# Performance work log

Measured on AMD Instinct MI355X. Metric: run time of the kernel, lower is better.

## Reference

```python
import jax, jax.numpy as jnp
import numpy as np

B, N, F_DIM = 32, 1024, 128
ALPHA = 0.2        # LeakyReLU negative slope
PAD = -9e15        # pad_sequence padding value in the original
DENSITY = 0.05


def setup_inputs() -> dict:
    key = jax.random.key(0)
    k1, k2, k3 = jax.random.split(key, 3)
    # sparse 0/1 adjacency with self-loops so every node has degree >= 1
    adj = (jax.random.uniform(k1, (B, N, N)) < DENSITY).astype(jnp.float32)
    eye = jnp.eye(N, dtype=jnp.float32)[None, :, :]
    adj = jnp.maximum(adj, eye)
    feats = jax.random.normal(k2, (B, N, F_DIM), dtype=jnp.float32)
    # xavier_uniform with leaky_relu gain on a [2F, 1]
    gain = float(np.sqrt(2.0 / (1.0 + ALPHA ** 2)))
    bound = gain * float(np.sqrt(6.0 / (2 * F_DIM + 1)))
    a = jax.random.uniform(k3, (2 * F_DIM, 1), minval=-bound, maxval=bound,
                           dtype=jnp.float32)
    return {"batch_graphs": adj, "batch_features": feats, "a": a}


def reference(batch_graphs, batch_features, a):
    # e_ij = LeakyReLU([h_i || h_j] @ a) decomposes as (h_i @ a1) + (h_j @ a2)
    s_src = batch_features @ a[:F_DIM, 0]   # [B, N] contribution of node i
    s_dst = batch_features @ a[F_DIM:, 0]   # [B, N] contribution of neighbor j
    e = s_src[:, :, None] + s_dst[:, None, :]            # [B, N, N]
    e = jnp.where(e >= 0, e, ALPHA * e)                   # LeakyReLU
    mask = batch_graphs == 1
    e = jnp.where(mask, e, PAD)                           # pad non-edges like pad_sequence
    att = jax.nn.softmax(e, axis=-1)                      # segmented softmax over neighbors
    att = jnp.where(mask, att, 0.0)                       # scatter back only real edges
    return att
```

## Files before the change

kernel.cpp:

```cpp
#include <hip/hip_runtime.h>
#include <hip/hip_bf16.h>
#include <stdint.h>

#define B_DIM 32
#define N_DIM 1024
#define F_DIM 128
#define ALPHA 0.2f
#define NROWS (B_DIM * N_DIM)
#define TAIL_ROWS 128
#define MAIN_ROWS (NROWS - TAIL_ROWS)
#define SCORE_BYTES ((size_t)(2 * NROWS) * sizeof(float))

typedef float          vf4 __attribute__((ext_vector_type(4)));
typedef unsigned short vh4 __attribute__((ext_vector_type(4)));

__device__ __forceinline__ unsigned short f32_to_bf16_bits(float f) {
    union { __hip_bfloat16 h; unsigned short u; } cvt;
    cvt.h = __float2bfloat16(f);
    return cvt.u;
}

__device__ __forceinline__ bool probe_is_f32(const void* adj) {
    return *(const uint32_t*)adj == 0x3F800000u;
}

template <bool F32>
__device__ __forceinline__ float* score_base(void* out) {
    const size_t out_bytes = (size_t)NROWS * N_DIM * (F32 ? 4 : 2);
    return (float*)((char*)out + out_bytes - SCORE_BYTES);
}

template <bool F32>
__device__ __forceinline__ void scores_body(
    const void* __restrict__ feats_v, const void* __restrict__ a_v, void* out)
{
    float* base  = score_base<F32>(out);
    float* s_src = base;
    float* s_dst = base + NROWS;

    const int wid  = threadIdx.x >> 6;
    const int lane = threadIdx.x & 63;
    const int row  = blockIdx.x * 4 + wid;
    const int f0   = lane * 2;

    float x0, x1, a10, a11, a20, a21;
    if (F32) {
        const float* fp = (const float*)feats_v + (size_t)row * F_DIM + f0;
        const float* ap = (const float*)a_v;
        x0 = fp[0]; x1 = fp[1];
        a10 = ap[f0];         a11 = ap[f0 + 1];
        a20 = ap[F_DIM + f0]; a21 = ap[F_DIM + f0 + 1];
    } else {
        const __hip_bfloat16* fp = (const __hip_bfloat16*)feats_v + (size_t)row * F_DIM + f0;
        const __hip_bfloat16* ap = (const __hip_bfloat16*)a_v;
        x0  = __bfloat162float(fp[0]);           x1  = __bfloat162float(fp[1]);
        a10 = __bfloat162float(ap[f0]);          a11 = __bfloat162float(ap[f0 + 1]);
        a20 = __bfloat162float(ap[F_DIM + f0]);  a21 = __bfloat162float(ap[F_DIM + f0 + 1]);
    }

    float v1 = x0 * a10 + x1 * a11;
    float v2 = x0 * a20 + x1 * a21;
    #pragma unroll
    for (int off = 32; off > 0; off >>= 1) {
        v1 += __shfl_down(v1, off, 64);
        v2 += __shfl_down(v2, off, 64);
    }
    if (lane == 0) { s_src[row] = v1; s_dst[row] = v2; }
}

__global__ __launch_bounds__(256) void scores_kernel(
    const void* __restrict__ adj, const void* __restrict__ feats,
    const void* __restrict__ a, void* out)
{
    if (probe_is_f32(adj)) scores_body<true>(feats, a, out);
    else                   scores_body<false>(feats, a, out);
}

template <bool F32>
__device__ __forceinline__ void wave_softmax_row(
    const void* __restrict__ adj_v, void* __restrict__ out_v,
    int row, float ssrc, const float* __restrict__ sdst )
{
    const int lane = threadIdx.x & 63;

    float p[16];
    float lsum = 0.0f;

    #pragma unroll
    for (int c = 0; c < 4; ++c) {
        const int idx = c * 64 + lane;
        const vf4 sd = ((const vf4*)sdst)[idx];
        float av[4];
        if (F32) {
            const vf4 aq = ((const vf4*)((const float*)adj_v + (size_t)row * N_DIM))[idx];
            av[0] = aq.x; av[1] = aq.y; av[2] = aq.z; av[3] = aq.w;
        } else {
            const vh4 aq = ((const vh4*)((const __hip_bfloat16*)adj_v + (size_t)row * N_DIM))[idx];
            av[0] = __uint_as_float((unsigned)aq.x << 16);
            av[1] = __uint_as_float((unsigned)aq.y << 16);
            av[2] = __uint_as_float((unsigned)aq.z << 16);
            av[3] = __uint_as_float((unsigned)aq.w << 16);
        }
        const float sdk[4] = {sd.x, sd.y, sd.z, sd.w};
        #pragma unroll
        for (int k = 0; k < 4; ++k) {
            float t = ssrc + sdk[k];
            t = fmaxf(t, ALPHA * t);
            const float e = __expf(t) * av[k];
            p[c * 4 + k] = e;
            lsum += e;
        }
    }

    #pragma unroll
    for (int off = 1; off < 64; off <<= 1)
        lsum += __shfl_xor(lsum, off, 64);
    const float inv = 1.0f / lsum;

    #pragma unroll
    for (int c = 0; c < 4; ++c) {
        const int idx = c * 64 + lane;
        if (F32) {
            vf4 o;
            o.x = p[c*4+0] * inv; o.y = p[c*4+1] * inv;
            o.z = p[c*4+2] * inv; o.w = p[c*4+3] * inv;
            ((vf4*)((float*)out_v + (size_t)row * N_DIM))[idx] = o;
        } else {
            vh4 o;
            o.x = f32_to_bf16_bits(p[c*4+0] * inv);
            o.y = f32_to_bf16_bits(p[c*4+1] * inv);
            o.z = f32_to_bf16_bits(p[c*4+2] * inv);
            o.w = f32_to_bf16_bits(p[c*4+3] * inv);
            ((vh4*)((__hip_bfloat16*)out_v + (size_t)row * N_DIM))[idx] = o;
        }
    }
}

template <bool F32>
__device__ __forceinline__ void main_body(const void* __restrict__ adj_v, void* out_v)
{
    const int wid = threadIdx.x >> 6;
    const int row = blockIdx.x * 4 + wid;
    const int b   = row >> 10;

    const float* base = score_base<F32>(out_v);
    const float  ssrc = base[row];
    const float* sdst = base + NROWS + (size_t)b * N_DIM;

    wave_softmax_row<F32>(adj_v, out_v, row, ssrc, sdst);
}

__global__ __launch_bounds__(256) void main_kernel(
    const void* __restrict__ adj, void* out)
{
    if (probe_is_f32(adj)) main_body<true>(adj, out);
    else                   main_body<false>(adj, out);
}

template <bool F32>
__device__ __forceinline__ void tail_body(
    const void* __restrict__ adj_v, const void* __restrict__ feats_v,
    const void* __restrict__ a_v, void* __restrict__ out_v)
{
    __shared__ float sdst_sh[N_DIM];

    const int tid  = threadIdx.x;
    const int wid  = tid >> 6;
    const int lane = tid & 63;
    const int b    = B_DIM - 1;
    const int row  = MAIN_ROWS + blockIdx.x * 4 + wid;

    #pragma unroll
    for (int k = 0; k < 4; ++k) {
        const int j = tid * 4 + k;
        float acc = 0.0f;
        if (F32) {
            const vf4* fp = (const vf4*)((const float*)feats_v + ((size_t)b * N_DIM + j) * F_DIM);
            const vf4* ap = (const vf4*)((const float*)a_v + F_DIM);
            #pragma unroll 8
            for (int f = 0; f < F_DIM / 4; ++f) {
                const vf4 x = fp[f], w = ap[f];
                acc += x.x * w.x + x.y * w.y + x.z * w.z + x.w * w.w;
            }
        } else {
            const __hip_bfloat16* fp = (const __hip_bfloat16*)feats_v + ((size_t)b * N_DIM + j) * F_DIM;
            const __hip_bfloat16* ap = (const __hip_bfloat16*)a_v + F_DIM;
            #pragma unroll 8
            for (int f = 0; f < F_DIM; ++f)
                acc += __bfloat162float(fp[f]) * __bfloat162float(ap[f]);
        }
        sdst_sh[j] = acc;
    }

    float ssrc;
    {
        const int f0 = lane * 2;
        float x0, x1, a0, a1;
        if (F32) {
            const float* fp = (const float*)feats_v + (size_t)row * F_DIM + f0;
            const float* ap = (const float*)a_v;
            x0 = fp[0]; x1 = fp[1]; a0 = ap[f0]; a1 = ap[f0 + 1];
        } else {
            const __hip_bfloat16* fp = (const __hip_bfloat16*)feats_v + (size_t)row * F_DIM + f0;
            const __hip_bfloat16* ap = (const __hip_bfloat16*)a_v;
            x0 = __bfloat162float(fp[0]); x1 = __bfloat162float(fp[1]);
            a0 = __bfloat162float(ap[f0]); a1 = __bfloat162float(ap[f0 + 1]);
        }
        float v = x0 * a0 + x1 * a1;
        #pragma unroll
        for (int off = 32; off > 0; off >>= 1)
            v += __shfl_down(v, off, 64);
        ssrc = __shfl(v, 0, 64);
    }
    __syncthreads();

    wave_softmax_row<F32>(adj_v, out_v, row, ssrc, sdst_sh);
}

__global__ __launch_bounds__(256) void tail_kernel(
    const void* __restrict__ adj, const void* __restrict__ feats,
    const void* __restrict__ a, void* __restrict__ out)
{
    if (probe_is_f32(adj)) tail_body<true>(adj, feats, a, out);
    else                   tail_body<false>(adj, feats, a, out);
}

extern "C" void kernel_launch(void* const* d_in, const int* in_sizes, int n_in,
                              void* d_out, int out_size, void* d_ws, size_t ws_size,
                              hipStream_t stream) {
    const void* adj   = d_in[0];
    const void* feats = d_in[1];
    const void* a     = d_in[2];
    (void)d_ws; (void)ws_size;

    scores_kernel<<<NROWS / 4, 256, 0, stream>>>(adj, feats, a, d_out);
    main_kernel<<<MAIN_ROWS / 4, 256, 0, stream>>>(adj, d_out);
    tail_kernel<<<TAIL_ROWS / 4, 256, 0, stream>>>(adj, feats, a, d_out);
}
```

Baseline: 263.3 us.

## Process four rows per wave with double-buffered adjacency loads and recomputed exponentials

The main softmax kernel now gives each wave four consecutive rows. It loads the shared s_dst slice once and double-buffers the adjacency-row loads, so the next row's loads are in flight while the current row is processed. Exponentials are recomputed in the store pass instead of being held in a 16-element array, which lowers register pressure, and the launch bound asks for higher occupancy. The scores kernel now handles two rows per wave with vector loads. The aim is better memory-latency hiding and less redundant s_dst traffic, at the cost of fewer blocks and doubled exp work.

```diff
diff --git a/kernel.cpp b/kernel.cpp
--- a/kernel.cpp
+++ b/kernel.cpp
@@ -40,32 +40,38 @@
 
     const int wid  = threadIdx.x >> 6;
     const int lane = threadIdx.x & 63;
-    const int row  = blockIdx.x * 4 + wid;
-    const int f0   = lane * 2;
-
-    float x0, x1, a10, a11, a20, a21;
+    const int pr   = blockIdx.x * 4 + wid;
+    const int row  = pr * 2 + (lane >> 5);
+    const int f0   = (lane & 31) * 4;
+
+    float x0, x1, x2, x3, w10, w11, w12, w13, w20, w21, w22, w23;
     if (F32) {
-        const float* fp = (const float*)feats_v + (size_t)row * F_DIM + f0;
-        const float* ap = (const float*)a_v;
-        x0 = fp[0]; x1 = fp[1];
-        a10 = ap[f0];         a11 = ap[f0 + 1];
-        a20 = ap[F_DIM + f0]; a21 = ap[F_DIM + f0 + 1];
+        const vf4 xv  = *(const vf4*)((const float*)feats_v + (size_t)row * F_DIM + f0);
+        const vf4 w1v = *(const vf4*)((const float*)a_v + f0);
+        const vf4 w2v = *(const vf4*)((const float*)a_v + F_DIM + f0);
+        x0 = xv.x;  x1 = xv.y;  x2 = xv.z;  x3 = xv.w;
+        w10 = w1v.x; w11 = w1v.y; w12 = w1v.z; w13 = w1v.w;
+        w20 = w2v.x; w21 = w2v.y; w22 = w2v.z; w23 = w2v.w;
     } else {
-        const __hip_bfloat16* fp = (const __hip_bfloat16*)feats_v + (size_t)row * F_DIM + f0;
-        const __hip_bfloat16* ap = (const __hip_bfloat16*)a_v;
-        x0  = __bfloat162float(fp[0]);           x1  = __bfloat162float(fp[1]);
-        a10 = __bfloat162float(ap[f0]);          a11 = __bfloat162float(ap[f0 + 1]);
-        a20 = __bfloat162float(ap[F_DIM + f0]);  a21 = __bfloat162float(ap[F_DIM + f0 + 1]);
-    }
-
-    float v1 = x0 * a10 + x1 * a11;
-    float v2 = x0 * a20 + x1 * a21;
-    #pragma unroll
-    for (int off = 32; off > 0; off >>= 1) {
-        v1 += __shfl_down(v1, off, 64);
-        v2 += __shfl_down(v2, off, 64);
-    }
-    if (lane == 0) { s_src[row] = v1; s_dst[row] = v2; }
+        const vh4 xv  = *(const vh4*)((const __hip_bfloat16*)feats_v + (size_t)row * F_DIM + f0);
+        const vh4 w1v = *(const vh4*)((const __hip_bfloat16*)a_v + f0);
+        const vh4 w2v = *(const vh4*)((const __hip_bfloat16*)a_v + F_DIM + f0);
+        x0 = __uint_as_float((unsigned)xv.x << 16);  x1 = __uint_as_float((unsigned)xv.y << 16);
+        x2 = __uint_as_float((unsigned)xv.z << 16);  x3 = __uint_as_float((unsigned)xv.w << 16);
+        w10 = __uint_as_float((unsigned)w1v.x << 16); w11 = __uint_as_float((unsigned)w1v.y << 16);
+        w12 = __uint_as_float((unsigned)w1v.z << 16); w13 = __uint_as_float((unsigned)w1v.w << 16);
+        w20 = __uint_as_float((unsigned)w2v.x << 16); w21 = __uint_as_float((unsigned)w2v.y << 16);
+        w22 = __uint_as_float((unsigned)w2v.z << 16); w23 = __uint_as_float((unsigned)w2v.w << 16);
+    }
+
+    float v1 = x0 * w10 + x1 * w11 + x2 * w12 + x3 * w13;
+    float v2 = x0 * w20 + x1 * w21 + x2 * w22 + x3 * w23;
+    #pragma unroll
+    for (int off = 1; off < 32; off <<= 1) {
+        v1 += __shfl_xor(v1, off, 64);
+        v2 += __shfl_xor(v2, off, 64);
+    }
+    if ((lane & 31) == 0) { s_src[row] = v1; s_dst[row] = v2; }
 }
 
 __global__ __launch_bounds__(256) void scores_kernel(
@@ -76,42 +82,40 @@
     else                   scores_body<false>(feats, a, out);
 }
 
-template <bool F32>
-__device__ __forceinline__ void wave_softmax_row(
-    const void* __restrict__ adj_v, void* __restrict__ out_v,
-    int row, float ssrc, const float* __restrict__ sdst )
-{
-    const int lane = threadIdx.x & 63;
-
-    float p[16];
+__device__ __forceinline__ float qget(const vf4& q, int k) { return q[k]; }
+__device__ __forceinline__ float qget(const vh4& q, int k) {
+    return __uint_as_float((unsigned)q[k] << 16);
+}
+
+template <bool F32> struct QSel  { using T = vf4; };
+template <>         struct QSel<false> { using T = vh4; };
+
+template <bool F32, class QV>
+__device__ __forceinline__ void load_adj_row(
+    const void* __restrict__ adj_v, int row, int lane, QV q[4])
+{
+    const QV* a0 = F32
+        ? (const QV*)((const float*)adj_v + (size_t)row * N_DIM)
+        : (const QV*)((const __hip_bfloat16*)adj_v + (size_t)row * N_DIM);
+    #pragma unroll
+    for (int c = 0; c < 4; ++c) q[c] = a0[c * 64 + lane];
+}
+
+template <bool F32, class QV>
+__device__ __forceinline__ void process_row(
+    void* __restrict__ out_v, int row, int lane, float ssrc,
+    const vf4 sd[4], const QV q[4])
+{
     float lsum = 0.0f;
-
     #pragma unroll
     for (int c = 0; c < 4; ++c) {
-        const int idx = c * 64 + lane;
-        const vf4 sd = ((const vf4*)sdst)[idx];
-        float av[4];
-        if (F32) {
-            const vf4 aq = ((const vf4*)((const float*)adj_v + (size_t)row * N_DIM))[idx];
-            av[0] = aq.x; av[1] = aq.y; av[2] = aq.z; av[3] = aq.w;
-        } else {
-            const vh4 aq = ((const vh4*)((const __hip_bfloat16*)adj_v + (size_t)row * N_DIM))[idx];
-            av[0] = __uint_as_float((unsigned)aq.x << 16);
-            av[1] = __uint_as_float((unsigned)aq.y << 16);
-            av[2] = __uint_as_float((unsigned)aq.z << 16);
-            av[3] = __uint_as_float((unsigned)aq.w << 16);
-        }
-        const float sdk[4] = {sd.x, sd.y, sd.z, sd.w};
         #pragma unroll
         for (int k = 0; k < 4; ++k) {
-            float t = ssrc + sdk[k];
+            float t = ssrc + sd[c][k];
             t = fmaxf(t, ALPHA * t);
-            const float e = __expf(t) * av[k];
-            p[c * 4 + k] = e;
-            lsum += e;
-        }
-    }
-
+            lsum += __expf(t) * qget(q[c], k);
+        }
+    }
     #pragma unroll
     for (int off = 1; off < 64; off <<= 1)
         lsum += __shfl_xor(lsum, off, 64);
@@ -122,15 +126,21 @@
         const int idx = c * 64 + lane;
         if (F32) {
             vf4 o;
-            o.x = p[c*4+0] * inv; o.y = p[c*4+1] * inv;
-            o.z = p[c*4+2] * inv; o.w = p[c*4+3] * inv;
+            #pragma unroll
+            for (int k = 0; k < 4; ++k) {
+                float t = ssrc + sd[c][k];
+                t = fmaxf(t, ALPHA * t);
+                o[k] = __expf(t) * qget(q[c], k) * inv;
+            }
             ((vf4*)((float*)out_v + (size_t)row * N_DIM))[idx] = o;
         } else {
             vh4 o;
-            o.x = f32_to_bf16_bits(p[c*4+0] * inv);
-            o.y = f32_to_bf16_bits(p[c*4+1] * inv);
-            o.z = f32_to_bf16_bits(p[c*4+2] * inv);
-            o.w = f32_to_bf16_bits(p[c*4+3] * inv);
+            #pragma unroll
+            for (int k = 0; k < 4; ++k) {
+                float t = ssrc + sd[c][k];
+                t = fmaxf(t, ALPHA * t);
+                o[k] = f32_to_bf16_bits(__expf(t) * qget(q[c], k) * inv);
+            }
             ((vh4*)((__hip_bfloat16*)out_v + (size_t)row * N_DIM))[idx] = o;
         }
     }
@@ -139,18 +149,37 @@
 template <bool F32>
 __device__ __forceinline__ void main_body(const void* __restrict__ adj_v, void* out_v)
 {
-    const int wid = threadIdx.x >> 6;
-    const int row = blockIdx.x * 4 + wid;
-    const int b   = row >> 10;
+    using QV = typename QSel<F32>::T;
+
+    const int wid  = threadIdx.x >> 6;
+    const int lane = threadIdx.x & 63;
+    const int gw   = blockIdx.x * 4 + wid;
+    const int r0   = gw * 4;
+    const int b    = r0 >> 10;
 
     const float* base = score_base<F32>(out_v);
-    const float  ssrc = base[row];
+    const float s0 = base[r0];
+    const float s1 = base[r0 + 1];
+    const float s2 = base[r0 + 2];
+    const float s3 = base[r0 + 3];
     const float* sdst = base + NROWS + (size_t)b * N_DIM;
 
-    wave_softmax_row<F32>(adj_v, out_v, row, ssrc, sdst);
-}
-
-__global__ __launch_bounds__(256) void main_kernel(
+    vf4 sd[4];
+    #pragma unroll
+    for (int c = 0; c < 4; ++c) sd[c] = ((const vf4*)sdst)[c * 64 + lane];
+
+    QV qa[4], qb[4];
+    load_adj_row<F32>(adj_v, r0,     lane, qa);
+    load_adj_row<F32>(adj_v, r0 + 1, lane, qb);
+    process_row<F32>(out_v, r0,     lane, s0, sd, qa);
+    load_adj_row<F32>(adj_v, r0 + 2, lane, qa);
+    process_row<F32>(out_v, r0 + 1, lane, s1, sd, qb);
+    load_adj_row<F32>(adj_v, r0 + 3, lane, qb);
+    process_row<F32>(out_v, r0 + 2, lane, s2, sd, qa);
+    process_row<F32>(out_v, r0 + 3, lane, s3, sd, qb);
+}
+
+__global__ __launch_bounds__(256, 8) void main_kernel(
     const void* __restrict__ adj, void* out)
 {
     if (probe_is_f32(adj)) main_body<true>(adj, out);
@@ -214,7 +243,13 @@
     }
     __syncthreads();
 
-    wave_softmax_row<F32>(adj_v, out_v, row, ssrc, sdst_sh);
+    using QV = typename QSel<F32>::T;
+    QV q[4];
+    load_adj_row<F32>(adj_v, row, lane, q);
+    vf4 sd[4];
+    #pragma unroll
+    for (int c = 0; c < 4; ++c) sd[c] = ((const vf4*)sdst_sh)[c * 64 + lane];
+    process_row<F32>(out_v, row, lane, ssrc, sd, q);
 }
 
 __global__ __launch_bounds__(256) void tail_kernel(
@@ -233,7 +268,7 @@
     const void* a     = d_in[2];
     (void)d_ws; (void)ws_size;
 
-    scores_kernel<<<NROWS / 4, 256, 0, stream>>>(adj, feats, a, d_out);
-    main_kernel<<<MAIN_ROWS / 4, 256, 0, stream>>>(adj, d_out);
+    scores_kernel<<<NROWS / 8, 256, 0, stream>>>(adj, feats, a, d_out);
+    main_kernel<<<MAIN_ROWS / 16, 256, 0, stream>>>(adj, d_out);
     tail_kernel<<<TAIL_ROWS / 4, 256, 0, stream>>>(adj, feats, a, d_out);
 }
```

Result: slower. 273.4 us (+3.8%).
